# Optimization experiments

Measured on AMD Instinct MI355X. Metric: run time of the kernel, lower is better.

Reference implementation:

```python
import jax, jax.numpy as jnp
import numpy as np

VOCAB, EMB, H1, H2, T, B = 21, 128, 64, 100, 500, 1024


def lstm(x, W_ih, W_hh, b_ih, b_hh):
    # x: [B, T, D]; torch gate order i, f, g, o
    Bx, H = x.shape[0], W_hh.shape[1]
    xproj = jnp.einsum('btd,gd->btg', x, W_ih) + b_ih  # [B, T, 4H]

    def step(carry, xt):
        h, c = carry
        gates = xt + h @ W_hh.T + b_hh
        i, f, g, o = jnp.split(gates, 4, axis=-1)
        c = jax.nn.sigmoid(f) * c + jax.nn.sigmoid(i) * jnp.tanh(g)
        h = jax.nn.sigmoid(o) * jnp.tanh(c)
        return (h, c), h

    h0 = jnp.zeros((Bx, H), x.dtype)
    _, hs = jax.lax.scan(step, (h0, h0), xproj.transpose(1, 0, 2))
    return hs.transpose(1, 0, 2)  # [B, T, H]


def setup_inputs() -> dict:
    key = jax.random.key(0)
    ks = jax.random.split(key, 12)
    s = 0.05
    x_idx = jax.random.randint(ks[0], (B, T), 0, VOCAB, dtype=jnp.int32)
    emb_table = jax.random.normal(ks[1], (VOCAB, EMB), jnp.float32) * s
    emb_table = emb_table.at[0].set(0.0)  # padding_idx=0
    d = dict(
        x_idx=x_idx,
        emb_table=emb_table,
        W_ih1=jax.random.normal(ks[2], (4 * H1, EMB), jnp.float32) * s,
        W_hh1=jax.random.normal(ks[3], (4 * H1, H1), jnp.float32) * s,
        b_ih1=jax.random.normal(ks[4], (4 * H1,), jnp.float32) * s,
        b_hh1=jax.random.normal(ks[5], (4 * H1,), jnp.float32) * s,
        W_ih2=jax.random.normal(ks[6], (4 * H2, H1), jnp.float32) * s,
        W_hh2=jax.random.normal(ks[7], (4 * H2, H2), jnp.float32) * s,
        b_ih2=jax.random.normal(ks[8], (4 * H2,), jnp.float32) * s,
        b_hh2=jax.random.normal(ks[9], (4 * H2,), jnp.float32) * s,
        fc_w=jax.random.normal(ks[10], (1, H2), jnp.float32) * s,
        fc_b=jax.random.normal(ks[11], (1,), jnp.float32) * s,
    )
    return d


def reference(x_idx, emb_table, W_ih1, W_hh1, b_ih1, b_hh1,
              W_ih2, W_hh2, b_ih2, b_hh2, fc_w, fc_b):
    # embedding with padding_idx=0 (row is zero; mask keeps grads faithful)
    x = emb_table[x_idx] * (x_idx != 0)[..., None].astype(emb_table.dtype)  # [B,T,128]
    x = lstm(x, W_ih1, W_hh1, b_ih1, b_hh1)  # [B,T,64]
    # MaxPool1d(kernel=5, stride=5) over time
    Bx, Tx, D = x.shape
    Tp = Tx // 5
    x = x[:, :Tp * 5].reshape(Bx, Tp, 5, D).max(axis=2)  # [B,T/5,64]
    x = lstm(x, W_ih2, W_hh2, b_ih2, b_hh2)  # [B,T/5,100]
    h = x[:, -1, :]
    return jax.nn.sigmoid(h @ fc_w.T + fc_b)  # [B,1]
```

## Files before the change

### kernel.cpp

```cpp
#include <hip/hip_runtime.h>

#define VOCAB 21
#define EMB 128
#define H1 64
#define H2 100
#define T1 500
#define TP 100
#define NB 1024
#define TBL_LD 260
#define LOG2E 1.44269504f

typedef __attribute__((ext_vector_type(8))) short bf16x8;
typedef __attribute__((ext_vector_type(4))) float f32x4;

__device__ __forceinline__ unsigned short f2bf(float x){
    union { float f; unsigned u; } v; v.f = x;
    return (unsigned short)((v.u + 0x8000u) >> 16);
}
__device__ __forceinline__ void bar_lds(){
    asm volatile("s_waitcnt lgkmcnt(0)\n\ts_barrier" ::: "memory");
}
__device__ __forceinline__ void wait_lds(){
    asm volatile("s_waitcnt lgkmcnt(0)" ::: "memory");
}
__device__ __forceinline__ float ex2(float x){ return __builtin_amdgcn_exp2f(x); }
__device__ __forceinline__ float rcp(float x){ return __builtin_amdgcn_rcpf(x); }

__global__ void k_table(const float* __restrict__ Wih, const float* __restrict__ emb,
                        const float* __restrict__ bih, const float* __restrict__ bhh,
                        float* __restrict__ table){
    const int p = threadIdx.x;
    const int v = blockIdx.x;
    const int orig = (p & 3) * H1 + (p >> 2);
    float s = bih[orig] + bhh[orig];
    if (v != 0){
        const float* w = Wih + orig * EMB;
        const float* e = emb + v * EMB;
        #pragma unroll 16
        for (int d = 0; d < EMB; ++d) s += w[d]*e[d];
    }
    table[v*TBL_LD + p] = s * LOG2E;
}

__global__ __launch_bounds__(1024, 1) void k_lstm1(
    const int* __restrict__ xidx, const float* __restrict__ Whh,
    const float* __restrict__ tbl_g, float* __restrict__ x2){
  __shared__ __align__(16) float table[VOCAB*TBL_LD];
  __shared__ __align__(16) unsigned short hbuf[2][16*64];
  __shared__ int idxs[16*T1];

  const int tid = threadIdx.x;
  const int gt = tid >> 6, l = tid & 63;
  const int b0 = blockIdx.x * 16;
  const int row = l & 15, kg = l >> 4;

  for (int i = tid; i < VOCAB*TBL_LD; i += 1024) table[i] = tbl_g[i];
  for (int i = tid; i < 16*T1; i += 1024){
      int r = i / T1, t = i - r*T1;
      idxs[i] = xidx[(b0 + r)*T1 + t];
  }
  { unsigned short* hz = (unsigned short*)hbuf;
    for (int i = tid; i < 2048; i += 1024) hz[i] = 0; }

  bf16x8 af0, af1;
  {
      const int p = 16*gt + row;
      const int orig = (p & 3)*H1 + (p >> 2);
      bf16x8 f;
      const float* s0 = Whh + orig*H1 + kg*8;
      #pragma unroll
      for (int j = 0; j < 8; ++j) f[j] = (short)f2bf(s0[j] * LOG2E);
      af0 = f;
      const float* s1 = Whh + orig*H1 + 32 + kg*8;
      #pragma unroll
      for (int j = 0; j < 8; ++j) f[j] = (short)f2bf(s1[j] * LOG2E);
      af1 = f;
  }

  char* hb = (char*)hbuf;
  const int swz = (row & 7) << 4;
  const int rb0 = (row*128 + 16*kg) ^ swz;
  const int rb1 = (row*128 + 64 + 16*kg) ^ swz;
  const int cell = 4*gt + kg;
  const int wbh  = (row*128 + 2*cell) ^ swz;
  const float twoL = 2.0f * LOG2E;

  float cc = 0.f, pm = -1e30f;
  __syncthreads();

  int vv = idxs[row*T1];
  f32x4 tq = *(const f32x4*)&table[vv*TBL_LD + 4*cell];
  int vnext = idxs[row*T1 + 1];

  int rp = 0, tm = 0, tp = 0;
  for (int t = 0; t < T1; ++t){
      bf16x8 bf0 = *(const bf16x8*)(hb + rp + rb0);
      bf16x8 bf1 = *(const bf16x8*)(hb + rp + rb1);
      f32x4 a = __builtin_amdgcn_mfma_f32_16x16x32_bf16(af0, bf0, tq, 0,0,0);
      f32x4 z = __builtin_amdgcn_mfma_f32_16x16x32_bf16(af1, bf1, a, 0,0,0);
      f32x4 tqn = *(const f32x4*)&table[vnext*TBL_LD + 4*cell];
      int vn2 = idxs[row*T1 + ((t + 2 < T1) ? (t + 2) : 0)];
      float si = rcp(1.f + ex2(-z[0]));
      float sf = rcp(1.f + ex2(-z[1]));
      float so = rcp(1.f + ex2(-z[3]));
      float tg = 1.f - 2.f*rcp(1.f + ex2(z[2] + z[2]));
      cc = sf*cc + si*tg;
      float th = 1.f - 2.f*rcp(1.f + ex2(twoL*cc));
      float h = so*th;
      const int wp = rp ^ 2048;
      *(unsigned short*)(hb + wp + wbh) = f2bf(h);
      pm = fmaxf(pm, h);
      if (++tm == 5){
          x2[(b0 + row)*(TP*H1) + tp*H1 + cell] = pm;
          pm = -1e30f; tm = 0; ++tp;
      }
      tq = tqn; vnext = vn2;
      rp = wp;
      bar_lds();
  }
}

__global__ __launch_bounds__(512, 1) void k_lstm2(
    const float* __restrict__ x2, const float* __restrict__ Wih,
    const float* __restrict__ Whh, const float* __restrict__ bih,
    const float* __restrict__ bhh, const float* __restrict__ fcw,
    const float* __restrict__ fcb, float* __restrict__ out){
  __shared__ __align__(16) unsigned short blds[2][16*192];
  __shared__ __align__(16) f32x4 gl2[108*4];
  __shared__ float fcred[8][4];

  const int tid = threadIdx.x;
  const int w = tid >> 6, l = tid & 63;
  const int b0 = blockIdx.x * 4;
  const int n = l & 15, kg = l >> 4;
  const int tlo = (w < 2) ? 4*w : 8 + 3*(w - 2);
  const int nt  = (w < 2) ? 4 : 3;

  { unsigned* bz0 = (unsigned*)blds;
    for (int i = tid; i < 3072; i += 512) bz0[i] = 0; }
  { float* gz = (float*)gl2;
    for (int i = tid; i < 432*4; i += 512) gz[i] = 0.f; }

  bf16x8 af[4][6];
  #pragma unroll
  for (int u = 0; u < 4; ++u){
      if (u < nt){
          const int p = 16*(tlo + u) + n;
          const int cell_ = p >> 2, gate = p & 3;
          #pragma unroll
          for (int c = 0; c < 6; ++c){
              bf16x8 f;
              #pragma unroll
              for (int jj = 0; jj < 8; ++jj){
                  int k = c*32 + kg*8 + jj;
                  float vv = 0.f;
                  if (cell_ < H2){
                      if (k < 64)           vv = Wih[(gate*H2 + cell_)*H1 + k];
                      else if (k < 64 + H2) vv = Whh[(gate*H2 + cell_)*H2 + (k - 64)];
                  }
                  f[jj] = (short)f2bf(vv * LOG2E);
              }
              af[u][c] = f;
          }
      }
  }

  f32x4 bz[4];
  #pragma unroll
  for (int u = 0; u < 4; ++u){
      const int cu = 4*(tlo + u) + kg;
      f32x4 b = {0.f,0.f,0.f,0.f};
      if (u < nt && cu < H2){
          #pragma unroll
          for (int g = 0; g < 4; ++g) b[g] = (bih[g*H2 + cu] + bhh[g*H2 + cu]) * LOG2E;
      }
      bz[u] = b;
  }

  const bool act = (l >> 2) < 4*nt;
  const int cellc = 4*tlo + (l >> 2);
  const int r_c = l & 3;
  const float fwv = (act && cellc < H2) ? fcw[cellc] : 0.f;
  const float twoL = 2.0f * LOG2E;

  char* bb = (char*)blds;
  char* gb = (char*)gl2;
  const int swz = (n & 7) << 4;
  int rb[6];
  #pragma unroll
  for (int c = 0; c < 6; ++c) rb[c] = (n*384 + 64*c + 16*kg) ^ swz;
  const int wbh = (r_c*384 + 2*(64 + cellc)) ^ (r_c << 4);

  const int xr = (tid >> 5) & 3, xc = tid & 31;
  const int xwb = (xr*384 + 4*xc) ^ (xr << 4);
  if (tid >= 384){
      float2 v = *(const float2*)&x2[(b0 + xr)*(TP*H1) + 2*xc];
      unsigned pk = (unsigned)f2bf(v.x) | ((unsigned)f2bf(v.y) << 16);
      *(unsigned*)(bb + xwb) = pk;
  }
  float cc = 0.f, hv = 0.f;
  __syncthreads();

  int rp = 0;
  for (int t = 0; t < TP; ++t){
      float2 xn = {0.f, 0.f};
      if (tid >= 384 && t + 1 < TP)
          xn = *(const float2*)&x2[(b0 + xr)*(TP*H1) + (t+1)*H1 + 2*xc];
      bf16x8 bf[6];
      #pragma unroll
      for (int c = 0; c < 6; ++c) bf[c] = *(const bf16x8*)(bb + rp + rb[c]);
      #pragma unroll
      for (int u = 0; u < 4; ++u){
          if (u < nt){
              f32x4 za = __builtin_amdgcn_mfma_f32_16x16x32_bf16(af[u][0], bf[0], bz[u], 0,0,0);
              f32x4 zb = __builtin_amdgcn_mfma_f32_16x16x32_bf16(af[u][1], bf[1], (f32x4){0.f,0.f,0.f,0.f}, 0,0,0);
              za = __builtin_amdgcn_mfma_f32_16x16x32_bf16(af[u][2], bf[2], za, 0,0,0);
              zb = __builtin_amdgcn_mfma_f32_16x16x32_bf16(af[u][3], bf[3], zb, 0,0,0);
              za = __builtin_amdgcn_mfma_f32_16x16x32_bf16(af[u][4], bf[4], za, 0,0,0);
              zb = __builtin_amdgcn_mfma_f32_16x16x32_bf16(af[u][5], bf[5], zb, 0,0,0);
              f32x4 z = za + zb;
              if (n < 4)
                  *(f32x4*)(gb + 256*(tlo + u) + 64*kg + 16*n) = z;
          }
      }
      wait_lds();
      const int wp = rp ^ 6144;
      if (act){
          f32x4 q = *(const f32x4*)(gb + 256*tlo + 16*l);
          float si = rcp(1.f + ex2(-q[0]));
          float sf = rcp(1.f + ex2(-q[1]));
          float so = rcp(1.f + ex2(-q[3]));
          float tg = 1.f - 2.f*rcp(1.f + ex2(q[2] + q[2]));
          cc = sf*cc + si*tg;
          float th = 1.f - 2.f*rcp(1.f + ex2(twoL*cc));
          hv = so*th;
          *(unsigned short*)(bb + wp + wbh) = f2bf(hv);
      }
      if (tid >= 384 && t + 1 < TP){
          unsigned pk = (unsigned)f2bf(xn.x) | ((unsigned)f2bf(xn.y) << 16);
          *(unsigned*)(bb + wp + xwb) = pk;
      }
      rp = wp;
      bar_lds();
  }

  float p = (act && cellc < H2) ? hv * fwv : 0.f;
  p += __shfl_xor(p, 4);
  p += __shfl_xor(p, 8);
  p += __shfl_xor(p, 16);
  p += __shfl_xor(p, 32);
  if (l < 4) fcred[w][l] = p;
  __syncthreads();
  if (tid < 4){
      float s = 0.f;
      #pragma unroll
      for (int ww = 0; ww < 8; ++ww) s += fcred[ww][tid];
      s += fcb[0];
      out[b0 + tid] = rcp(1.f + ex2(-s * LOG2E));
  }
}

extern "C" void kernel_launch(void* const* d_in, const int* in_sizes, int n_in,
                              void* d_out, int out_size, void* d_ws, size_t ws_size,
                              hipStream_t stream) {
    const int*   x_idx = (const int*)  d_in[0];
    const float* emb   = (const float*)d_in[1];
    const float* Wih1  = (const float*)d_in[2];
    const float* Whh1  = (const float*)d_in[3];
    const float* bih1  = (const float*)d_in[4];
    const float* bhh1  = (const float*)d_in[5];
    const float* Wih2  = (const float*)d_in[6];
    const float* Whh2  = (const float*)d_in[7];
    const float* bih2  = (const float*)d_in[8];
    const float* bhh2  = (const float*)d_in[9];
    const float* fcw   = (const float*)d_in[10];
    const float* fcb   = (const float*)d_in[11];
    float* out = (float*)d_out;

    float* table = (float*)d_ws;
    float* x2    = (float*)((char*)d_ws + 32768);

    k_table<<<VOCAB, 256, 0, stream>>>(Wih1, emb, bih1, bhh1, table);
    k_lstm1<<<NB / 16, 1024, 0, stream>>>(x_idx, Whh1, table, x2);
    k_lstm2<<<NB / 4, 512, 0, stream>>>(x2, Wih2, Whh2, bih2, bhh2, fcw, fcb, out);
}
```

Before: 320.8 us.

## Store pooled layer-1 output as bf16 and feed MFMA operands from registers

Result: faster. 305.7 us (-4.7%).

```diff
diff --git a/kernel.cpp b/kernel.cpp
--- a/kernel.cpp
+++ b/kernel.cpp
@@ -44,7 +44,7 @@
 
 __global__ __launch_bounds__(1024, 1) void k_lstm1(
     const int* __restrict__ xidx, const float* __restrict__ Whh,
-    const float* __restrict__ tbl_g, float* __restrict__ x2){
+    const float* __restrict__ tbl_g, unsigned short* __restrict__ x2b){
   __shared__ __align__(16) float table[VOCAB*TBL_LD];
   __shared__ __align__(16) unsigned short hbuf[2][16*64];
   __shared__ int idxs[16*T1];
@@ -111,7 +111,7 @@
       *(unsigned short*)(hb + wp + wbh) = f2bf(h);
       pm = fmaxf(pm, h);
       if (++tm == 5){
-          x2[(b0 + row)*(TP*H1) + tp*H1 + cell] = pm;
+          x2b[(b0 + row)*(TP*H1) + tp*H1 + cell] = f2bf(pm);
           pm = -1e30f; tm = 0; ++tp;
       }
       tq = tqn; vnext = vn2;
@@ -121,11 +121,11 @@
 }
 
 __global__ __launch_bounds__(512, 1) void k_lstm2(
-    const float* __restrict__ x2, const float* __restrict__ Wih,
+    const unsigned short* __restrict__ x2b, const float* __restrict__ Wih,
     const float* __restrict__ Whh, const float* __restrict__ bih,
     const float* __restrict__ bhh, const float* __restrict__ fcw,
     const float* __restrict__ fcb, float* __restrict__ out){
-  __shared__ __align__(16) unsigned short blds[2][16*192];
+  __shared__ __align__(16) unsigned short blds[2][16*128];
   __shared__ __align__(16) f32x4 gl2[108*4];
   __shared__ float fcred[8][4];
 
@@ -136,8 +136,8 @@
   const int tlo = (w < 2) ? 4*w : 8 + 3*(w - 2);
   const int nt  = (w < 2) ? 4 : 3;
 
-  { unsigned* bz0 = (unsigned*)blds;
-    for (int i = tid; i < 3072; i += 512) bz0[i] = 0; }
+  { unsigned short* bz0 = (unsigned short*)blds;
+    for (int i = tid; i < 4096; i += 512) bz0[i] = 0; }
   { float* gz = (float*)gl2;
     for (int i = tid; i < 432*4; i += 512) gz[i] = 0.f; }
 
@@ -185,46 +185,46 @@
 
   char* bb = (char*)blds;
   char* gb = (char*)gl2;
-  const int swz = (n & 7) << 4;
-  int rb[6];
+  int rbh[4];
   #pragma unroll
-  for (int c = 0; c < 6; ++c) rb[c] = (n*384 + 64*c + 16*kg) ^ swz;
-  const int wbh = (r_c*384 + 2*(64 + cellc)) ^ (r_c << 4);
-
-  const int xr = (tid >> 5) & 3, xc = tid & 31;
-  const int xwb = (xr*384 + 4*xc) ^ (xr << 4);
-  if (tid >= 384){
-      float2 v = *(const float2*)&x2[(b0 + xr)*(TP*H1) + 2*xc];
-      unsigned pk = (unsigned)f2bf(v.x) | ((unsigned)f2bf(v.y) << 16);
-      *(unsigned*)(bb + xwb) = pk;
-  }
+  for (int j = 0; j < 4; ++j)
+      rbh[j] = (n*256 + 2*(j*32 + 8*kg)) ^ ((n & 7) << 4);
+  const int wbh = (r_c*256 + 2*cellc) ^ ((r_c & 7) << 4);
+
+  const int nr = n & 3;
+  const unsigned short* xrow = x2b + (b0 + nr)*(TP*H1) + kg*8;
+  bf16x8 x0 = *(const bf16x8*)(xrow);
+  bf16x8 x1 = *(const bf16x8*)(xrow + 32);
   float cc = 0.f, hv = 0.f;
   __syncthreads();
 
   int rp = 0;
   for (int t = 0; t < TP; ++t){
-      float2 xn = {0.f, 0.f};
-      if (tid >= 384 && t + 1 < TP)
-          xn = *(const float2*)&x2[(b0 + xr)*(TP*H1) + (t+1)*H1 + 2*xc];
-      bf16x8 bf[6];
-      #pragma unroll
-      for (int c = 0; c < 6; ++c) bf[c] = *(const bf16x8*)(bb + rp + rb[c]);
+      bf16x8 xn0, xn1;
+      if (t + 1 < TP){
+          xn0 = *(const bf16x8*)(xrow + (t+1)*H1);
+          xn1 = *(const bf16x8*)(xrow + (t+1)*H1 + 32);
+      }
+      bf16x8 h0 = *(const bf16x8*)(bb + rp + rbh[0]);
+      bf16x8 h1 = *(const bf16x8*)(bb + rp + rbh[1]);
+      bf16x8 h2 = *(const bf16x8*)(bb + rp + rbh[2]);
+      bf16x8 h3 = *(const bf16x8*)(bb + rp + rbh[3]);
       #pragma unroll
       for (int u = 0; u < 4; ++u){
           if (u < nt){
-              f32x4 za = __builtin_amdgcn_mfma_f32_16x16x32_bf16(af[u][0], bf[0], bz[u], 0,0,0);
-              f32x4 zb = __builtin_amdgcn_mfma_f32_16x16x32_bf16(af[u][1], bf[1], (f32x4){0.f,0.f,0.f,0.f}, 0,0,0);
-              za = __builtin_amdgcn_mfma_f32_16x16x32_bf16(af[u][2], bf[2], za, 0,0,0);
-              zb = __builtin_amdgcn_mfma_f32_16x16x32_bf16(af[u][3], bf[3], zb, 0,0,0);
-              za = __builtin_amdgcn_mfma_f32_16x16x32_bf16(af[u][4], bf[4], za, 0,0,0);
-              zb = __builtin_amdgcn_mfma_f32_16x16x32_bf16(af[u][5], bf[5], zb, 0,0,0);
+              f32x4 za = __builtin_amdgcn_mfma_f32_16x16x32_bf16(af[u][0], x0, bz[u], 0,0,0);
+              f32x4 zb = __builtin_amdgcn_mfma_f32_16x16x32_bf16(af[u][1], x1, (f32x4){0.f,0.f,0.f,0.f}, 0,0,0);
+              za = __builtin_amdgcn_mfma_f32_16x16x32_bf16(af[u][2], h0, za, 0,0,0);
+              zb = __builtin_amdgcn_mfma_f32_16x16x32_bf16(af[u][3], h1, zb, 0,0,0);
+              za = __builtin_amdgcn_mfma_f32_16x16x32_bf16(af[u][4], h2, za, 0,0,0);
+              zb = __builtin_amdgcn_mfma_f32_16x16x32_bf16(af[u][5], h3, zb, 0,0,0);
               f32x4 z = za + zb;
               if (n < 4)
                   *(f32x4*)(gb + 256*(tlo + u) + 64*kg + 16*n) = z;
           }
       }
       wait_lds();
-      const int wp = rp ^ 6144;
+      const int wp = rp ^ 4096;
       if (act){
           f32x4 q = *(const f32x4*)(gb + 256*tlo + 16*l);
           float si = rcp(1.f + ex2(-q[0]));
@@ -236,10 +236,7 @@
           hv = so*th;
           *(unsigned short*)(bb + wp + wbh) = f2bf(hv);
       }
-      if (tid >= 384 && t + 1 < TP){
-          unsigned pk = (unsigned)f2bf(xn.x) | ((unsigned)f2bf(xn.y) << 16);
-          *(unsigned*)(bb + wp + xwb) = pk;
-      }
+      x0 = xn0; x1 = xn1;
       rp = wp;
       bar_lds();
   }
@@ -277,10 +274,10 @@
     const float* fcb   = (const float*)d_in[11];
     float* out = (float*)d_out;
 
-    float* table = (float*)d_ws;
-    float* x2    = (float*)((char*)d_ws + 32768);
+    float*          table = (float*)d_ws;
+    unsigned short* x2b   = (unsigned short*)((char*)d_ws + 32768);
 
     k_table<<<VOCAB, 256, 0, stream>>>(Wih1, emb, bih1, bhh1, table);
-    k_lstm1<<<NB / 16, 1024, 0, stream>>>(x_idx, Whh1, table, x2);
-    k_lstm2<<<NB / 4, 512, 0, stream>>>(x2, Wih2, Whh2, bih2, bhh2, fcw, fcb, out);
-}
+    k_lstm1<<<NB / 16, 1024, 0, stream>>>(x_idx, Whh1, table, x2b);
+    k_lstm2<<<NB / 4, 512, 0, stream>>>(x2b, Wih2, Whh2, bih2, bhh2, fcw, fcb, out);
+}
```
